# Kernel tuning notes

Measured on AMD Instinct MI355X. Metric: run time of the kernel, lower is better.

## Reference

```python
import jax, jax.numpy as jnp
import numpy as np

N_RAYS = 4096
N_SAMPLES = 128
NEAR, FAR = 0.5, 4.0
BOX_MIN, BOX_MAX = -4.0, 4.0
N_LEVELS = 16
F_PER_LEVEL = 2
LOG2_T = 19
LOW_RES, HIGH_RES = 16.0, 512.0
GEO_FEAT = 15
HIDDEN = 64
HIDDEN_C = 64
IN_CH = N_LEVELS * F_PER_LEVEL      # 32 hash-grid features
IN_CH_VIEWS = 16                     # SH degree 4
OUT_CH = 4                           # 3 color channels + sigma (last)
N_APP = 64
APP_DIM = 16

PRIMES = np.array([1, 2654435761, 805459861], dtype=np.uint32)
OFFSETS = np.array([[i, j, k] for i in (0, 1) for j in (0, 1) for k in (0, 1)], dtype=np.int32)  # [8,3]

C0 = 0.28209479177387814
C1 = 0.4886025119029199
C2 = (1.0925484305920792, -1.0925484305920792, 0.31539156525252005, -1.0925484305920792, 0.5462742152960396)
C3 = (-0.5900435899266435, 2.890611442640554, -0.4570457994644658, 0.3731763325901154, -0.4570457994644658, 1.445305721320277, -0.5900435899266435)


def sh_encode(d):
    x, y, z = d[..., 0], d[..., 1], d[..., 2]
    xx, yy, zz = x * x, y * y, z * z
    xy, yz, xz = x * y, y * z, x * z
    return jnp.stack([
        C0 * jnp.ones_like(x),
        -C1 * y, C1 * z, -C1 * x,
        C2[0] * xy, C2[1] * yz, C2[2] * (2 * zz - xx - yy), C2[3] * xz, C2[4] * (xx - yy),
        C3[0] * y * (3 * xx - yy), C3[1] * xy * z, C3[2] * y * (4 * zz - xx - yy),
        C3[3] * z * (2 * zz - 3 * xx - 3 * yy), C3[4] * x * (4 * zz - xx - yy),
        C3[5] * z * (xx - yy), C3[6] * x * (xx - 3 * yy)], axis=-1)


def hash_encode(x, tables):
    # x: [N,3]; tables: [L, 2^T, F]. Multi-res hash grid with trilinear interp (Instant-NGP / HashNeRF).
    keep = jnp.all((x >= BOX_MIN) & (x <= BOX_MAX), axis=-1)
    xc = jnp.clip(x, BOX_MIN, BOX_MAX)
    b = np.exp((np.log(HIGH_RES) - np.log(LOW_RES)) / (N_LEVELS - 1))
    resolutions = jnp.asarray(np.floor(LOW_RES * b ** np.arange(N_LEVELS)), dtype=jnp.float32)
    hmask = jnp.uint32(2 ** LOG2_T - 1)
    primes = jnp.asarray(PRIMES)
    off = jnp.asarray(OFFSETS)
    off_u = off.astype(jnp.uint32)

    def level(args):
        table, res = args
        grid = (BOX_MAX - BOX_MIN) / res
        pos = (xc - BOX_MIN) / grid
        bl = jnp.floor(pos)
        frac = pos - bl                                    # [N,3]
        corners = bl.astype(jnp.uint32)[:, None, :] + off_u[None]  # [N,8,3]
        h = corners * primes                               # uint32 wraparound
        idx = (h[..., 0] ^ h[..., 1] ^ h[..., 2]) & hmask  # [N,8]
        emb = table[idx]                                   # [N,8,F]
        w = jnp.stack([1.0 - frac, frac], axis=-1)         # [N,3,2]
        cw = w[:, 0, off[:, 0]] * w[:, 1, off[:, 1]] * w[:, 2, off[:, 2]]  # [N,8]
        return jnp.einsum('nc,ncf->nf', cw, emb)           # [N,F]

    feats = jax.lax.map(level, (tables, resolutions))      # [L,N,F]
    feats = jnp.transpose(feats, (1, 0, 2)).reshape(x.shape[0], -1)
    return feats, keep


def _forward(rays, hash_tables, w_s0, w_s1, w_s2, w_c0, w_c1, w_c2, w_c3, app_table):
    R = rays.shape[0]
    rays_o, rays_d = rays[:, :3], rays[:, 3:6]
    codes = rays[:, 6].astype(jnp.int32)
    z = jnp.linspace(NEAR, FAR, N_SAMPLES)
    zvals = jax.lax.stop_gradient(jnp.broadcast_to(z, (R, N_SAMPLES)))
    samples = jax.lax.stop_gradient(rays_o[:, None, :] + rays_d[:, None, :] * z[None, :, None])  # [R,S,3]
    viewdirs = jax.lax.stop_gradient(jnp.broadcast_to(rays_d[:, None, :], (R, N_SAMPLES, 3)))

    pts = samples.reshape(-1, 3)
    dirs = viewdirs.reshape(-1, 3)
    enc_p, keep = hash_encode(pts, hash_tables)            # [N,32], [N]
    enc_d = sh_encode(dirs)                                # [N,16]

    # sigma network (bias-free, HashNeRF NeRFSmall)
    h = jax.nn.relu(enc_p @ w_s0)
    h = jax.nn.relu(h @ w_s1)
    h = h @ w_s2                                           # [N, 1+geo_feat]
    sigma = h[:, :1]
    geo = h[:, 1:]

    # color network with per-ray appearance embedding
    app = app_table[jnp.repeat(codes, N_SAMPLES)]          # [N, APP_DIM]
    c = jnp.concatenate([enc_d, geo, app], axis=-1)
    c = jax.nn.relu(c @ w_c0)
    c = jax.nn.relu(c @ w_c1)
    c = jax.nn.relu(c @ w_c2)
    c = c @ w_c3                                           # [N, OUT_CH-1]

    sigma = jnp.where(keep[:, None], sigma, 0.0)           # output[~keep_mask, -1] = 0
    raw = jnp.concatenate([c, sigma], axis=-1).reshape(R, N_SAMPLES, OUT_CH)

    # volumetric integration
    dists = jnp.concatenate([zvals[:, 1:] - zvals[:, :-1], jnp.full((R, 1), 1e10)], axis=-1)
    dists = dists * jnp.linalg.norm(rays_d, axis=-1, keepdims=True)
    sig = jax.nn.relu(raw[..., -1])
    alpha = 1.0 - jnp.exp(-sig * dists)
    trans = jnp.cumprod(jnp.concatenate([jnp.ones((R, 1)), 1.0 - alpha + 1e-10], axis=-1), axis=-1)[:, :-1]
    weights = alpha * trans                                # [R,S]
    chs = jax.nn.sigmoid(raw[..., :-1])
    chs_map = jnp.einsum('rs,rsc->rc', weights, chs)       # [R, OUT_CH-1]
    depth_map = jnp.sum(weights * zvals, axis=-1)          # [R]
    p = jnp.concatenate([weights, 1.0 - jnp.sum(weights, -1, keepdims=True) + 1e-6], axis=-1)
    p = jnp.clip(p, 1e-12, None)
    p = p / jnp.sum(p, -1, keepdims=True)
    sparsity_loss = -jnp.sum(p * jnp.log(p), axis=-1)      # [R] Categorical entropy
    return chs_map, depth_map, sparsity_loss


def setup_inputs() -> dict:
    key = jax.random.key(0)
    ks = jax.random.split(key, 12)
    rays_o = jax.random.uniform(ks[0], (N_RAYS, 3), minval=-0.5, maxval=0.5)
    d = jax.random.normal(ks[1], (N_RAYS, 3))
    rays_d = d / jnp.linalg.norm(d, axis=-1, keepdims=True)
    codes = jax.random.randint(ks[2], (N_RAYS, 1), 0, N_APP).astype(jnp.float32)
    rays = jnp.concatenate([rays_o, rays_d, codes], axis=-1)  # [R,7]
    hash_tables = (jax.random.uniform(ks[3], (N_LEVELS, 2 ** LOG2_T, F_PER_LEVEL)) * 2.0 - 1.0) * 1e-4
    def init_w(k, shape):
        return jax.random.normal(k, shape) * (1.0 / np.sqrt(shape[0]))
    w_s0 = init_w(ks[4], (IN_CH, HIDDEN))
    w_s1 = init_w(ks[5], (HIDDEN, HIDDEN))
    w_s2 = init_w(ks[6], (HIDDEN, 1 + GEO_FEAT))
    c_in = IN_CH_VIEWS + GEO_FEAT + APP_DIM
    w_c0 = init_w(ks[7], (c_in, HIDDEN_C))
    w_c1 = init_w(ks[8], (HIDDEN_C, HIDDEN_C))
    w_c2 = init_w(ks[9], (HIDDEN_C, HIDDEN_C))
    w_c3 = init_w(ks[10], (HIDDEN_C, OUT_CH - 1))
    app_table = jax.random.normal(ks[11], (N_APP, APP_DIM)) * 0.01
    return {"rays": rays, "app_code": 0, "hash_tables": hash_tables,
            "w_s0": w_s0, "w_s1": w_s1, "w_s2": w_s2,
            "w_c0": w_c0, "w_c1": w_c1, "w_c2": w_c2, "w_c3": w_c3,
            "app_table": app_table}


def reference(rays, app_code, hash_tables, w_s0, w_s1, w_s2, w_c0, w_c1, w_c2, w_c3, app_table):
    # app_code arg is ignored by the original forward (it re-reads rays[:, 6]).
    return _forward(rays, hash_tables, w_s0, w_s1, w_s2, w_c0, w_c1, w_c2, w_c3, app_table)
```

## Files before the change

kernel.cpp:

```cpp
#include <hip/hip_runtime.h>
#include <math.h>

typedef unsigned short u16;
typedef short bf16x8 __attribute__((ext_vector_type(8)));
typedef float f32x4 __attribute__((ext_vector_type(4)));

#define NRAYS 4096
#define NSAMP 128
#define NPTS (NRAYS * NSAMP)
#define TBL_MASK 0x7FFFFu
#define LVL_STRIDE (524288 * 2)

#define WB_C0 0
#define WB_C1 4096
#define WB_C2 8192
#define WB_C3 12288
#define RAW_OFF 65536

#define MEMBAR() asm volatile("" ::: "memory")

struct ResArr { float r[16]; };

__device__ __forceinline__ u16 f2b(float f) {
  unsigned u = __float_as_uint(f);
  unsigned r = u + 0x7FFFu + ((u >> 16) & 1u);
  return (u16)(r >> 16);
}
__device__ __forceinline__ unsigned pack2(float lo, float hi) {
  return (unsigned)f2b(lo) | ((unsigned)f2b(hi) << 16);
}
__device__ __forceinline__ float b2f(u16 u) {
  return __uint_as_float(((unsigned)u) << 16);
}
__device__ __forceinline__ float sigmoidf_(float x) { return 1.f / (1.f + expf(-x)); }

template<int IN, int OUT>
__device__ __forceinline__ void layer(const float (&in)[IN], float (&out)[OUT],
                                      const float* __restrict__ W, bool dorelu)
{
  constexpr int CH = (OUT < 32) ? OUT : 32;
  #pragma unroll
  for (int oc = 0; oc < OUT; oc += CH) {
    float acc[CH];
    #pragma unroll
    for (int o = 0; o < CH; ++o) acc[o] = 0.f;
    #pragma unroll
    for (int i = 0; i < IN; ++i) {
      const float x = in[i];
      const float* wr = W + i * OUT + oc;
      #pragma unroll
      for (int o = 0; o < CH; ++o) acc[o] = fmaf(x, wr[o], acc[o]);
    }
    #pragma unroll
    for (int o = 0; o < CH; ++o) out[oc + o] = dorelu ? fmaxf(acc[o], 0.f) : acc[o];
  }
}

__global__ void __launch_bounds__(256)
prep_kernel(const float* __restrict__ wc0, const float* __restrict__ wc1,
            const float* __restrict__ wc2, const float* __restrict__ wc3,
            u16* __restrict__ wb)
{
  __shared__ int P[32];
  __shared__ int Pinv[32];
  const int t = threadIdx.x;
  if (t < 64) {
    const int g = t >> 4;
    for (int tt = 0; tt < 32; ++tt) {
      bf16x8 A, B;
      #pragma unroll
      for (int e = 0; e < 8; ++e) {
        A[e] = (short)f2b((float)(g * 8 + e + 1));
        B[e] = (short)((g * 8 + e == tt) ? 0x3F80 : 0);
      }
      f32x4 c = {0.f, 0.f, 0.f, 0.f};
      c = __builtin_amdgcn_mfma_f32_16x16x32_bf16(A, B, c, 0, 0, 0);
      if (t == 0) P[tt] = (int)(c[0] + 0.5f) - 1;
    }
  }
  __syncthreads();
  if (t < 32) Pinv[t] = t;
  __syncthreads();
  if (t < 32) { int p = P[t]; if (p >= 0 && p < 32) Pinv[p] = t; }
  __syncthreads();

  for (int i = t; i < 4096; i += 256) {
    int o = i >> 6, s6 = i & 63, kt = (s6 & 32) | Pinv[s6 & 31];
    wb[WB_C0 + i] = f2b(kt < 47 ? wc0[kt * 64 + o] : 0.f);
  }
  for (int i = t; i < 4096; i += 256) {
    int o = i >> 6, s6 = i & 63, kt = (s6 & 32) | Pinv[s6 & 31];
    wb[WB_C1 + i] = f2b(wc1[kt * 64 + o]);
  }
  for (int i = t; i < 4096; i += 256) {
    int o = i >> 6, s6 = i & 63, kt = (s6 & 32) | Pinv[s6 & 31];
    wb[WB_C2 + i] = f2b(wc2[kt * 64 + o]);
  }
  for (int i = t; i < 1024; i += 256) {
    int o = i >> 6, s6 = i & 63, kt = (s6 & 32) | Pinv[s6 & 31];
    wb[WB_C3 + i] = f2b(o < 3 ? wc3[kt * 3 + o] : 0.f);
  }
}

__global__ void __launch_bounds__(256, 4)
point_kernel(const float* __restrict__ rays, const float* __restrict__ tables,
             const float* __restrict__ ws0, const float* __restrict__ ws1,
             const float* __restrict__ ws2, const u16* __restrict__ wb,
             const float* __restrict__ app_table, u16* __restrict__ raw, ResArr RES)
{
  __shared__ char lds[4 * 8192 + 4 * 64 * 4];
  const int t = threadIdx.x, wv = t >> 6, lane = t & 63;
  char* buf = lds + wv * 8192;
  float* sigb = (float*)(lds + 32768 + wv * 256);
  const int pBase = blockIdx.x * 256 + wv * 64;
  const int q = lane & 15, g = lane >> 4;
  const unsigned fswz = (unsigned)((q & 7) << 4);
  const unsigned myswz = (unsigned)((lane & 7) << 4);

  const int ptG = pBase + lane;
  const int r = ptG >> 7, s = ptG & (NSAMP - 1);
  const float ox = rays[r * 7 + 0], oy = rays[r * 7 + 1], oz = rays[r * 7 + 2];
  const float dx = rays[r * 7 + 3], dy = rays[r * 7 + 4], dz = rays[r * 7 + 5];
  const int code = (int)rays[r * 7 + 6];
  const float z = 0.5f + (3.5f / 127.f) * (float)s;
  const float x = fmaf(dx, z, ox), y = fmaf(dy, z, oy), w = fmaf(dz, z, oz);
  const bool keep = (x >= -4.f && x <= 4.f && y >= -4.f && y <= 4.f &&
                     w >= -4.f && w <= 4.f);
  const float xc = fminf(fmaxf(x, -4.f), 4.f);
  const float yc = fminf(fmaxf(y, -4.f), 4.f);
  const float zc = fminf(fmaxf(w, -4.f), 4.f);

  float encp[32];
  #pragma unroll
  for (int l = 0; l < 16; ++l) {
    const float res = RES.r[l];
    const float sc = res * 0.125f;
    const float px = (xc + 4.f) * sc, py = (yc + 4.f) * sc, pz = (zc + 4.f) * sc;
    const float bx = floorf(px), by = floorf(py), bz = floorf(pz);
    const float fx = px - bx, fy = py - by, fz = pz - bz;
    const unsigned ix = (unsigned)bx, iy = (unsigned)by, iz = (unsigned)bz;
    const unsigned hx0 = ix, hx1 = ix + 1u;
    const unsigned hy0 = iy * 2654435761u, hy1 = (iy + 1u) * 2654435761u;
    const unsigned hz0 = iz * 805459861u,  hz1 = (iz + 1u) * 805459861u;
    const float wx0 = 1.f - fx, wy0 = 1.f - fy, wz0 = 1.f - fz;
    const float* tl = tables + (size_t)l * LVL_STRIDE;
    float f0 = 0.f, f1 = 0.f;
    #pragma unroll
    for (int c = 0; c < 8; ++c) {
      const unsigned cx = (c >> 2) & 1, cy = (c >> 1) & 1, cz = c & 1;
      const unsigned idx = ((cx ? hx1 : hx0) ^ (cy ? hy1 : hy0) ^ (cz ? hz1 : hz0)) & TBL_MASK;
      const float cw = (cx ? fx : wx0) * (cy ? fy : wy0) * (cz ? fz : wz0);
      const float2 e = *reinterpret_cast<const float2*>(tl + (size_t)idx * 2);
      f0 = fmaf(cw, e.x, f0);
      f1 = fmaf(cw, e.y, f1);
    }
    encp[2 * l] = f0;
    encp[2 * l + 1] = f1;
  }

  float h1[64]; layer<32, 64>(encp, h1, ws0, true);
  float h2[64]; layer<64, 64>(h1, h2, ws1, true);
  float gg[16]; layer<64, 16>(h2, gg, ws2, false);
  sigb[lane] = keep ? gg[0] : 0.f;

  {
    float cin[64];
    const float xx = dx * dx, yy = dy * dy, zz2 = dz * dz;
    const float xy = dx * dy, yz = dy * dz, xz = dx * dz;
    cin[0]  = 0.28209479177387814f;
    cin[1]  = -0.4886025119029199f * dy;
    cin[2]  = 0.4886025119029199f * dz;
    cin[3]  = -0.4886025119029199f * dx;
    cin[4]  = 1.0925484305920792f * xy;
    cin[5]  = -1.0925484305920792f * yz;
    cin[6]  = 0.31539156525252005f * (2.f * zz2 - xx - yy);
    cin[7]  = -1.0925484305920792f * xz;
    cin[8]  = 0.5462742152960396f * (xx - yy);
    cin[9]  = -0.5900435899266435f * dy * (3.f * xx - yy);
    cin[10] = 2.890611442640554f * xy * dz;
    cin[11] = -0.4570457994644658f * dy * (4.f * zz2 - xx - yy);
    cin[12] = 0.3731763325901154f * dz * (2.f * zz2 - 3.f * xx - 3.f * yy);
    cin[13] = -0.4570457994644658f * dx * (4.f * zz2 - xx - yy);
    cin[14] = 1.445305721320277f * dz * (xx - yy);
    cin[15] = -0.5900435899266435f * dx * (xx - 3.f * yy);
    #pragma unroll
    for (int i = 0; i < 15; ++i) cin[16 + i] = gg[1 + i];
    const float4* ap = (const float4*)(app_table + (size_t)code * 16);
    float4 a0 = ap[0], a1 = ap[1], a2 = ap[2], a3 = ap[3];
    cin[31] = a0.x; cin[32] = a0.y; cin[33] = a0.z; cin[34] = a0.w;
    cin[35] = a1.x; cin[36] = a1.y; cin[37] = a1.z; cin[38] = a1.w;
    cin[39] = a2.x; cin[40] = a2.y; cin[41] = a2.z; cin[42] = a2.w;
    cin[43] = a3.x; cin[44] = a3.y; cin[45] = a3.z; cin[46] = a3.w;
    #pragma unroll
    for (int i = 47; i < 64; ++i) cin[i] = 0.f;
    #pragma unroll
    for (int c = 0; c < 8; ++c) {
      uint4 u;
      u.x = pack2(cin[8 * c + 0], cin[8 * c + 1]);
      u.y = pack2(cin[8 * c + 2], cin[8 * c + 3]);
      u.z = pack2(cin[8 * c + 4], cin[8 * c + 5]);
      u.w = pack2(cin[8 * c + 6], cin[8 * c + 7]);
      *(uint4*)(buf + lane * 128 + (((unsigned)(c * 16)) ^ myswz)) = u;
    }
  }
  MEMBAR();

  auto rdB = [&](int n, int kc) -> bf16x8 {
    return *(const bf16x8*)(buf + (n * 16 + q) * 128 + (((unsigned)(kc * 64 + g * 16)) ^ fswz));
  };
  auto ldA = [&](const u16* Wp, int row, int kc) -> bf16x8 {
    return *(const bf16x8*)(Wp + row * 64 + kc * 32 + g * 8);
  };
  auto wrC = [&](int n, int slot0, f32x4 c) {
    c[0] = fmaxf(c[0], 0.f); c[1] = fmaxf(c[1], 0.f);
    c[2] = fmaxf(c[2], 0.f); c[3] = fmaxf(c[3], 0.f);
    uint2 u; u.x = pack2(c[0], c[1]); u.y = pack2(c[2], c[3]);
    *(uint2*)(buf + (n * 16 + q) * 128 + (((unsigned)(slot0 * 2)) ^ fswz)) = u;
  };

  auto layer64 = [&](const u16* Wp) {
    bf16x8 A[4][2];
    #pragma unroll
    for (int m = 0; m < 4; ++m) {
      A[m][0] = ldA(Wp, m * 16 + q, 0);
      A[m][1] = ldA(Wp, m * 16 + q, 1);
    }
    #pragma unroll
    for (int n = 0; n < 4; ++n) {
      bf16x8 b0 = rdB(n, 0), b1 = rdB(n, 1);
      #pragma unroll
      for (int m = 0; m < 4; ++m) {
        f32x4 c = f32x4{0.f, 0.f, 0.f, 0.f};
        c = __builtin_amdgcn_mfma_f32_16x16x32_bf16(A[m][0], b0, c, 0, 0, 0);
        c = __builtin_amdgcn_mfma_f32_16x16x32_bf16(A[m][1], b1, c, 0, 0, 0);
        wrC(n, m * 16 + g * 4, c);
      }
    }
    MEMBAR();
  };

  layer64(wb + WB_C0);
  layer64(wb + WB_C1);
  layer64(wb + WB_C2);

  {
    const u16* Wp = wb + WB_C3;
    bf16x8 A0 = ldA(Wp, q, 0), A1 = ldA(Wp, q, 1);
    #pragma unroll
    for (int n = 0; n < 4; ++n) {
      bf16x8 b0 = rdB(n, 0), b1 = rdB(n, 1);
      f32x4 c = f32x4{0.f, 0.f, 0.f, 0.f};
      c = __builtin_amdgcn_mfma_f32_16x16x32_bf16(A0, b0, c, 0, 0, 0);
      c = __builtin_amdgcn_mfma_f32_16x16x32_bf16(A1, b1, c, 0, 0, 0);
      if (g == 0) {
        uint2 o; o.x = pack2(c[0], c[1]); o.y = pack2(c[2], sigb[n * 16 + q]);
        *(uint2*)(raw + (size_t)(pBase + n * 16 + q) * 4) = o;
      }
    }
  }
}

__global__ void __launch_bounds__(256)
render_kernel(const float* __restrict__ rays, const u16* __restrict__ raw,
              float* __restrict__ out)
{
  const int r = blockIdx.x * 256 + threadIdx.x;
  if (r >= NRAYS) return;
  const float dx = rays[r * 7 + 3], dy = rays[r * 7 + 4], dz = rays[r * 7 + 5];
  const float nrm = sqrtf(dx * dx + dy * dy + dz * dz);
  const float dstep = 3.5f / 127.f;
  const ushort4* rp = reinterpret_cast<const ushort4*>(raw) + (size_t)r * NSAMP;

  float T = 1.f, sumw = 0.f, sumwz = 0.f, cm0 = 0.f, cm1 = 0.f, cm2 = 0.f;
  for (int s = 0; s < NSAMP; ++s) {
    const ushort4 rw = rp[s];
    const float dist = ((s < NSAMP - 1) ? dstep : 1e10f) * nrm;
    const float sigv = fmaxf(b2f(rw.w), 0.f);
    const float alpha = 1.f - expf(-sigv * dist);
    const float wgt = alpha * T;
    T *= (1.f - alpha + 1e-10f);
    const float zv = 0.5f + dstep * (float)s;
    sumw += wgt;
    sumwz = fmaf(wgt, zv, sumwz);
    cm0 = fmaf(wgt, sigmoidf_(b2f(rw.x)), cm0);
    cm1 = fmaf(wgt, sigmoidf_(b2f(rw.y)), cm1);
    cm2 = fmaf(wgt, sigmoidf_(b2f(rw.z)), cm2);
  }

  float S1 = 0.f, S2 = 0.f, T2 = 1.f;
  for (int s = 0; s < NSAMP; ++s) {
    const ushort4 rw = rp[s];
    const float dist = ((s < NSAMP - 1) ? dstep : 1e10f) * nrm;
    const float sigv = fmaxf(b2f(rw.w), 0.f);
    const float alpha = 1.f - expf(-sigv * dist);
    const float wgt = alpha * T2;
    T2 *= (1.f - alpha + 1e-10f);
    const float qv = fmaxf(wgt, 1e-12f);
    S1 += qv;
    S2 = fmaf(qv, logf(qv), S2);
  }
  const float plast = fmaxf(1.f - sumw + 1e-6f, 1e-12f);
  S1 += plast;
  S2 = fmaf(plast, logf(plast), S2);
  const float ent = logf(S1) - S2 / S1;

  out[r * 3 + 0] = cm0;
  out[r * 3 + 1] = cm1;
  out[r * 3 + 2] = cm2;
  out[NRAYS * 3 + r] = sumwz;
  out[NRAYS * 4 + r] = ent;
}

extern "C" void kernel_launch(void* const* d_in, const int* in_sizes, int n_in,
                              void* d_out, int out_size, void* d_ws, size_t ws_size,
                              hipStream_t stream)
{
  const float* rays   = (const float*)d_in[0];
  const float* tables = (const float*)d_in[2];
  const float* ws0    = (const float*)d_in[3];
  const float* ws1    = (const float*)d_in[4];
  const float* ws2    = (const float*)d_in[5];
  const float* wc0    = (const float*)d_in[6];
  const float* wc1    = (const float*)d_in[7];
  const float* wc2    = (const float*)d_in[8];
  const float* wc3    = (const float*)d_in[9];
  const float* app    = (const float*)d_in[10];

  u16* wb  = (u16*)d_ws;
  u16* raw = (u16*)((char*)d_ws + RAW_OFF);
  float* out = (float*)d_out;

  ResArr RES;
  const double b = exp((log(512.0) - log(16.0)) / 15.0);
  for (int l = 0; l < 16; ++l) RES.r[l] = (float)floor(16.0 * pow(b, (double)l));

  hipLaunchKernelGGL(prep_kernel, dim3(1), dim3(256), 0, stream,
                     wc0, wc1, wc2, wc3, wb);
  hipLaunchKernelGGL(point_kernel, dim3(NPTS / 256), dim3(256), 0, stream,
                     rays, tables, ws0, ws1, ws2, wb, app, raw, RES);
  hipLaunchKernelGGL(render_kernel, dim3(16), dim3(256), 0, stream,
                     rays, raw, out);
}
```

Baseline: 279.4 us.

## Move sigma MLP to MFMA with three-way bf16 split emulating fp32

The density MLP (32→64→64→16), previously evaluated with scalar fp32 FMAs per thread, now runs on bf16 MFMA. Weights and activations are each split into high/mid/low bf16 parts so the sum of cross products approximates fp32 accuracy. The geo-feature output is written straight into the LDS color-input buffer, with the color weights remapped around the sigma slot. This replaces heavy VALU work and register pressure with six-term MFMA passes and more LDS round-trips, and occupancy is lowered to 3 waves-blocks.

```diff
diff --git a/kernel.cpp b/kernel.cpp
--- a/kernel.cpp
+++ b/kernel.cpp
@@ -11,15 +11,25 @@
 #define TBL_MASK 0x7FFFFu
 #define LVL_STRIDE (524288 * 2)
 
-#define WB_C0 0
-#define WB_C1 4096
-#define WB_C2 8192
-#define WB_C3 12288
-#define RAW_OFF 65536
+#define SB_W0H 0
+#define SB_W0M 2048
+#define SB_W0L 4096
+#define SB_W1H 6144
+#define SB_W1M 10240
+#define SB_W1L 14336
+#define SB_W2H 18432
+#define SB_W2M 19456
+#define SB_W2L 20480
+#define WB_C0 21504
+#define WB_C1 25600
+#define WB_C2 29696
+#define WB_C3 33792
+#define RAW_OFF 131072
 
 #define MEMBAR() asm volatile("" ::: "memory")
 
 struct ResArr { float r[16]; };
+template<int N> struct IC { static constexpr int value = N; };
 
 __device__ __forceinline__ u16 f2b(float f) {
   unsigned u = __float_as_uint(f);
@@ -32,34 +42,22 @@
 __device__ __forceinline__ float b2f(u16 u) {
   return __uint_as_float(((unsigned)u) << 16);
 }
+template<int SP>
+__device__ __forceinline__ u16 splitb(float x) {
+  u16 h = f2b(x);
+  if (SP == 0) return h;
+  float r = x - b2f(h);
+  u16 m = f2b(r);
+  if (SP == 1) return m;
+  return f2b(r - b2f(m));
+}
 __device__ __forceinline__ float sigmoidf_(float x) { return 1.f / (1.f + expf(-x)); }
 
-template<int IN, int OUT>
-__device__ __forceinline__ void layer(const float (&in)[IN], float (&out)[OUT],
-                                      const float* __restrict__ W, bool dorelu)
-{
-  constexpr int CH = (OUT < 32) ? OUT : 32;
-  #pragma unroll
-  for (int oc = 0; oc < OUT; oc += CH) {
-    float acc[CH];
-    #pragma unroll
-    for (int o = 0; o < CH; ++o) acc[o] = 0.f;
-    #pragma unroll
-    for (int i = 0; i < IN; ++i) {
-      const float x = in[i];
-      const float* wr = W + i * OUT + oc;
-      #pragma unroll
-      for (int o = 0; o < CH; ++o) acc[o] = fmaf(x, wr[o], acc[o]);
-    }
-    #pragma unroll
-    for (int o = 0; o < CH; ++o) out[oc + o] = dorelu ? fmaxf(acc[o], 0.f) : acc[o];
-  }
-}
-
 __global__ void __launch_bounds__(256)
-prep_kernel(const float* __restrict__ wc0, const float* __restrict__ wc1,
-            const float* __restrict__ wc2, const float* __restrict__ wc3,
-            u16* __restrict__ wb)
+prep_kernel(const float* __restrict__ ws0, const float* __restrict__ ws1,
+            const float* __restrict__ ws2, const float* __restrict__ wc0,
+            const float* __restrict__ wc1, const float* __restrict__ wc2,
+            const float* __restrict__ wc3, u16* __restrict__ wb)
 {
   __shared__ int P[32];
   __shared__ int Pinv[32];
@@ -84,34 +82,81 @@
   if (t < 32) { int p = P[t]; if (p >= 0 && p < 32) Pinv[p] = t; }
   __syncthreads();
 
+  for (int i = t; i < 2048; i += 256) {
+    int o = i >> 5, k = i & 31, kt = Pinv[k];
+    float v = ws0[kt * 64 + o];
+    u16 h = f2b(v); float r = v - b2f(h); u16 m = f2b(r); u16 l = f2b(r - b2f(m));
+    wb[SB_W0H + i] = h; wb[SB_W0M + i] = m; wb[SB_W0L + i] = l;
+  }
   for (int i = t; i < 4096; i += 256) {
-    int o = i >> 6, s6 = i & 63, kt = (s6 & 32) | Pinv[s6 & 31];
-    wb[WB_C0 + i] = f2b(kt < 47 ? wc0[kt * 64 + o] : 0.f);
+    int o = i >> 6, k = i & 63, kt = (k & 32) | Pinv[k & 31];
+    float v = ws1[kt * 64 + o];
+    u16 h = f2b(v); float r = v - b2f(h); u16 m = f2b(r); u16 l = f2b(r - b2f(m));
+    wb[SB_W1H + i] = h; wb[SB_W1M + i] = m; wb[SB_W1L + i] = l;
+  }
+  for (int i = t; i < 1024; i += 256) {
+    int o = i >> 6, k = i & 63, kt = (k & 32) | Pinv[k & 31];
+    float v = ws2[kt * 16 + o];
+    u16 h = f2b(v); float r = v - b2f(h); u16 m = f2b(r); u16 l = f2b(r - b2f(m));
+    wb[SB_W2H + i] = h; wb[SB_W2M + i] = m; wb[SB_W2L + i] = l;
   }
   for (int i = t; i < 4096; i += 256) {
-    int o = i >> 6, s6 = i & 63, kt = (s6 & 32) | Pinv[s6 & 31];
+    int o = i >> 6, s = i & 63, kt = (s & 32) | Pinv[s & 31];
+    float v = 0.f;
+    if (kt < 16) v = wc0[kt * 64 + o];
+    else if (kt >= 17 && kt <= 47) v = wc0[(kt - 1) * 64 + o];
+    wb[WB_C0 + i] = f2b(v);
+  }
+  for (int i = t; i < 4096; i += 256) {
+    int o = i >> 6, s = i & 63, kt = (s & 32) | Pinv[s & 31];
     wb[WB_C1 + i] = f2b(wc1[kt * 64 + o]);
   }
   for (int i = t; i < 4096; i += 256) {
-    int o = i >> 6, s6 = i & 63, kt = (s6 & 32) | Pinv[s6 & 31];
+    int o = i >> 6, s = i & 63, kt = (s & 32) | Pinv[s & 31];
     wb[WB_C2 + i] = f2b(wc2[kt * 64 + o]);
   }
   for (int i = t; i < 1024; i += 256) {
-    int o = i >> 6, s6 = i & 63, kt = (s6 & 32) | Pinv[s6 & 31];
+    int o = i >> 6, s = i & 63, kt = (s & 32) | Pinv[s & 31];
     wb[WB_C3 + i] = f2b(o < 3 ? wc3[kt * 3 + o] : 0.f);
   }
 }
 
-__global__ void __launch_bounds__(256, 4)
+template<int NM, int NKC, int NASP>
+__device__ __forceinline__ void sigma_pass(const char* buf, const u16* __restrict__ wb,
+                                           int offH, int offM, int offL,
+                                           f32x4 (&acc)[4][NM], int q, int g, unsigned fswz)
+{
+  #pragma unroll
+  for (int n = 0; n < 4; ++n) {
+    bf16x8 b[NKC];
+    #pragma unroll
+    for (int kc = 0; kc < NKC; ++kc)
+      b[kc] = *(const bf16x8*)(buf + (n * 16 + q) * 128 + (((unsigned)(kc * 64 + g * 16)) ^ fswz));
+    #pragma unroll
+    for (int m = 0; m < NM; ++m) {
+      const int arow = (NM == 1 ? q : m * 16 + q);
+      #pragma unroll
+      for (int asp = 0; asp < NASP; ++asp) {
+        const u16* Wp = wb + (asp == 0 ? offH : (asp == 1 ? offM : offL));
+        #pragma unroll
+        for (int kc = 0; kc < NKC; ++kc) {
+          bf16x8 A = *(const bf16x8*)(Wp + arow * (NKC * 32) + kc * 32 + g * 8);
+          acc[n][m] = __builtin_amdgcn_mfma_f32_16x16x32_bf16(A, b[kc], acc[n][m], 0, 0, 0);
+        }
+      }
+    }
+  }
+}
+
+__global__ void __launch_bounds__(256, 3)
 point_kernel(const float* __restrict__ rays, const float* __restrict__ tables,
-             const float* __restrict__ ws0, const float* __restrict__ ws1,
-             const float* __restrict__ ws2, const u16* __restrict__ wb,
-             const float* __restrict__ app_table, u16* __restrict__ raw, ResArr RES)
+             const u16* __restrict__ wb, const float* __restrict__ app_table,
+             u16* __restrict__ raw, ResArr RES)
 {
-  __shared__ char lds[4 * 8192 + 4 * 64 * 4];
+  __shared__ char lds[4 * 8192 + 4 * 256];
   const int t = threadIdx.x, wv = t >> 6, lane = t & 63;
   char* buf = lds + wv * 8192;
-  float* sigb = (float*)(lds + 32768 + wv * 256);
+  float* keepb = (float*)(lds + 32768 + wv * 256);
   const int pBase = blockIdx.x * 256 + wv * 64;
   const int q = lane & 15, g = lane >> 4;
   const unsigned fswz = (unsigned)((q & 7) << 4);
@@ -157,51 +202,124 @@
     encp[2 * l] = f0;
     encp[2 * l + 1] = f1;
   }
-
-  float h1[64]; layer<32, 64>(encp, h1, ws0, true);
-  float h2[64]; layer<64, 64>(h1, h2, ws1, true);
-  float gg[16]; layer<64, 16>(h2, gg, ws2, false);
-  sigb[lane] = keep ? gg[0] : 0.f;
+  keepb[lane] = keep ? 1.f : 0.f;
+
+  auto fillEnc = [&](auto SPc) {
+    constexpr int SP = decltype(SPc)::value;
+    #pragma unroll
+    for (int c = 0; c < 4; ++c) {
+      uint4 u;
+      u.x = (unsigned)splitb<SP>(encp[8 * c + 0]) | ((unsigned)splitb<SP>(encp[8 * c + 1]) << 16);
+      u.y = (unsigned)splitb<SP>(encp[8 * c + 2]) | ((unsigned)splitb<SP>(encp[8 * c + 3]) << 16);
+      u.z = (unsigned)splitb<SP>(encp[8 * c + 4]) | ((unsigned)splitb<SP>(encp[8 * c + 5]) << 16);
+      u.w = (unsigned)splitb<SP>(encp[8 * c + 6]) | ((unsigned)splitb<SP>(encp[8 * c + 7]) << 16);
+      *(uint4*)(buf + lane * 128 + (((unsigned)(c * 16)) ^ myswz)) = u;
+    }
+  };
+  auto fillC = [&](const f32x4 (&a)[4][4], auto SPc) {
+    constexpr int SP = decltype(SPc)::value;
+    #pragma unroll
+    for (int n = 0; n < 4; ++n)
+      #pragma unroll
+      for (int m = 0; m < 4; ++m) {
+        uint2 u;
+        u.x = (unsigned)splitb<SP>(a[n][m][0]) | ((unsigned)splitb<SP>(a[n][m][1]) << 16);
+        u.y = (unsigned)splitb<SP>(a[n][m][2]) | ((unsigned)splitb<SP>(a[n][m][3]) << 16);
+        *(uint2*)(buf + (n * 16 + q) * 128 + (((unsigned)(m * 32 + g * 8)) ^ fswz)) = u;
+      }
+  };
+
+  f32x4 acc0[4][4];
+  #pragma unroll
+  for (int n = 0; n < 4; ++n)
+    #pragma unroll
+    for (int m = 0; m < 4; ++m) acc0[n][m] = f32x4{0.f, 0.f, 0.f, 0.f};
+
+  fillEnc(IC<0>{}); MEMBAR();
+  sigma_pass<4, 1, 3>(buf, wb, SB_W0H, SB_W0M, SB_W0L, acc0, q, g, fswz); MEMBAR();
+  fillEnc(IC<1>{}); MEMBAR();
+  sigma_pass<4, 1, 2>(buf, wb, SB_W0H, SB_W0M, SB_W0L, acc0, q, g, fswz); MEMBAR();
+  fillEnc(IC<2>{}); MEMBAR();
+  sigma_pass<4, 1, 1>(buf, wb, SB_W0H, SB_W0M, SB_W0L, acc0, q, g, fswz); MEMBAR();
+  #pragma unroll
+  for (int n = 0; n < 4; ++n)
+    #pragma unroll
+    for (int m = 0; m < 4; ++m)
+      #pragma unroll
+      for (int j = 0; j < 4; ++j) acc0[n][m][j] = fmaxf(acc0[n][m][j], 0.f);
+
+  f32x4 acc1[4][4];
+  #pragma unroll
+  for (int n = 0; n < 4; ++n)
+    #pragma unroll
+    for (int m = 0; m < 4; ++m) acc1[n][m] = f32x4{0.f, 0.f, 0.f, 0.f};
+
+  fillC(acc0, IC<0>{}); MEMBAR();
+  sigma_pass<4, 2, 3>(buf, wb, SB_W1H, SB_W1M, SB_W1L, acc1, q, g, fswz); MEMBAR();
+  fillC(acc0, IC<1>{}); MEMBAR();
+  sigma_pass<4, 2, 2>(buf, wb, SB_W1H, SB_W1M, SB_W1L, acc1, q, g, fswz); MEMBAR();
+  fillC(acc0, IC<2>{}); MEMBAR();
+  sigma_pass<4, 2, 1>(buf, wb, SB_W1H, SB_W1M, SB_W1L, acc1, q, g, fswz); MEMBAR();
+  #pragma unroll
+  for (int n = 0; n < 4; ++n)
+    #pragma unroll
+    for (int m = 0; m < 4; ++m)
+      #pragma unroll
+      for (int j = 0; j < 4; ++j) acc1[n][m][j] = fmaxf(acc1[n][m][j], 0.f);
+
+  f32x4 acc2[4][1];
+  #pragma unroll
+  for (int n = 0; n < 4; ++n) acc2[n][0] = f32x4{0.f, 0.f, 0.f, 0.f};
+
+  fillC(acc1, IC<0>{}); MEMBAR();
+  sigma_pass<1, 2, 3>(buf, wb, SB_W2H, SB_W2M, SB_W2L, acc2, q, g, fswz); MEMBAR();
+  fillC(acc1, IC<1>{}); MEMBAR();
+  sigma_pass<1, 2, 2>(buf, wb, SB_W2H, SB_W2M, SB_W2L, acc2, q, g, fswz); MEMBAR();
+  fillC(acc1, IC<2>{}); MEMBAR();
+  sigma_pass<1, 2, 1>(buf, wb, SB_W2H, SB_W2M, SB_W2L, acc2, q, g, fswz); MEMBAR();
+
+  float sigv[4];
+  #pragma unroll
+  for (int n = 0; n < 4; ++n) {
+    sigv[n] = acc2[n][0][0] * keepb[n * 16 + q];
+    uint2 u;
+    u.x = pack2(acc2[n][0][0], acc2[n][0][1]);
+    u.y = pack2(acc2[n][0][2], acc2[n][0][3]);
+    *(uint2*)(buf + (n * 16 + q) * 128 + (((unsigned)(32 + 8 * g)) ^ fswz)) = u;
+  }
 
   {
-    float cin[64];
     const float xx = dx * dx, yy = dy * dy, zz2 = dz * dz;
     const float xy = dx * dy, yz = dy * dz, xz = dx * dz;
-    cin[0]  = 0.28209479177387814f;
-    cin[1]  = -0.4886025119029199f * dy;
-    cin[2]  = 0.4886025119029199f * dz;
-    cin[3]  = -0.4886025119029199f * dx;
-    cin[4]  = 1.0925484305920792f * xy;
-    cin[5]  = -1.0925484305920792f * yz;
-    cin[6]  = 0.31539156525252005f * (2.f * zz2 - xx - yy);
-    cin[7]  = -1.0925484305920792f * xz;
-    cin[8]  = 0.5462742152960396f * (xx - yy);
-    cin[9]  = -0.5900435899266435f * dy * (3.f * xx - yy);
-    cin[10] = 2.890611442640554f * xy * dz;
-    cin[11] = -0.4570457994644658f * dy * (4.f * zz2 - xx - yy);
-    cin[12] = 0.3731763325901154f * dz * (2.f * zz2 - 3.f * xx - 3.f * yy);
-    cin[13] = -0.4570457994644658f * dx * (4.f * zz2 - xx - yy);
-    cin[14] = 1.445305721320277f * dz * (xx - yy);
-    cin[15] = -0.5900435899266435f * dx * (xx - 3.f * yy);
-    #pragma unroll
-    for (int i = 0; i < 15; ++i) cin[16 + i] = gg[1 + i];
+    float e0 = 0.28209479177387814f;
+    float e1 = -0.4886025119029199f * dy;
+    float e2 = 0.4886025119029199f * dz;
+    float e3 = -0.4886025119029199f * dx;
+    float e4 = 1.0925484305920792f * xy;
+    float e5 = -1.0925484305920792f * yz;
+    float e6 = 0.31539156525252005f * (2.f * zz2 - xx - yy);
+    float e7 = -1.0925484305920792f * xz;
+    float e8 = 0.5462742152960396f * (xx - yy);
+    float e9 = -0.5900435899266435f * dy * (3.f * xx - yy);
+    float e10 = 2.890611442640554f * xy * dz;
+    float e11 = -0.4570457994644658f * dy * (4.f * zz2 - xx - yy);
+    float e12 = 0.3731763325901154f * dz * (2.f * zz2 - 3.f * xx - 3.f * yy);
+    float e13 = -0.4570457994644658f * dx * (4.f * zz2 - xx - yy);
+    float e14 = 1.445305721320277f * dz * (xx - yy);
+    float e15 = -0.5900435899266435f * dx * (xx - 3.f * yy);
+    uint4 u0; u0.x = pack2(e0, e1);  u0.y = pack2(e2, e3);  u0.z = pack2(e4, e5);  u0.w = pack2(e6, e7);
+    uint4 u1; u1.x = pack2(e8, e9);  u1.y = pack2(e10, e11); u1.z = pack2(e12, e13); u1.w = pack2(e14, e15);
+    *(uint4*)(buf + lane * 128 + (0u ^ myswz)) = u0;
+    *(uint4*)(buf + lane * 128 + (16u ^ myswz)) = u1;
     const float4* ap = (const float4*)(app_table + (size_t)code * 16);
     float4 a0 = ap[0], a1 = ap[1], a2 = ap[2], a3 = ap[3];
-    cin[31] = a0.x; cin[32] = a0.y; cin[33] = a0.z; cin[34] = a0.w;
-    cin[35] = a1.x; cin[36] = a1.y; cin[37] = a1.z; cin[38] = a1.w;
-    cin[39] = a2.x; cin[40] = a2.y; cin[41] = a2.z; cin[42] = a2.w;
-    cin[43] = a3.x; cin[44] = a3.y; cin[45] = a3.z; cin[46] = a3.w;
-    #pragma unroll
-    for (int i = 47; i < 64; ++i) cin[i] = 0.f;
-    #pragma unroll
-    for (int c = 0; c < 8; ++c) {
-      uint4 u;
-      u.x = pack2(cin[8 * c + 0], cin[8 * c + 1]);
-      u.y = pack2(cin[8 * c + 2], cin[8 * c + 3]);
-      u.z = pack2(cin[8 * c + 4], cin[8 * c + 5]);
-      u.w = pack2(cin[8 * c + 6], cin[8 * c + 7]);
-      *(uint4*)(buf + lane * 128 + (((unsigned)(c * 16)) ^ myswz)) = u;
-    }
+    uint4 v0; v0.x = pack2(a0.x, a0.y); v0.y = pack2(a0.z, a0.w); v0.z = pack2(a1.x, a1.y); v0.w = pack2(a1.z, a1.w);
+    uint4 v1; v1.x = pack2(a2.x, a2.y); v1.y = pack2(a2.z, a2.w); v1.z = pack2(a3.x, a3.y); v1.w = pack2(a3.z, a3.w);
+    *(uint4*)(buf + lane * 128 + (64u ^ myswz)) = v0;
+    *(uint4*)(buf + lane * 128 + (80u ^ myswz)) = v1;
+    uint4 zv; zv.x = 0u; zv.y = 0u; zv.z = 0u; zv.w = 0u;
+    *(uint4*)(buf + lane * 128 + (96u ^ myswz)) = zv;
+    *(uint4*)(buf + lane * 128 + (112u ^ myswz)) = zv;
   }
   MEMBAR();
 
@@ -217,7 +335,6 @@
     uint2 u; u.x = pack2(c[0], c[1]); u.y = pack2(c[2], c[3]);
     *(uint2*)(buf + (n * 16 + q) * 128 + (((unsigned)(slot0 * 2)) ^ fswz)) = u;
   };
-
   auto layer64 = [&](const u16* Wp) {
     bf16x8 A[4][2];
     #pragma unroll
@@ -253,7 +370,7 @@
       c = __builtin_amdgcn_mfma_f32_16x16x32_bf16(A0, b0, c, 0, 0, 0);
       c = __builtin_amdgcn_mfma_f32_16x16x32_bf16(A1, b1, c, 0, 0, 0);
       if (g == 0) {
-        uint2 o; o.x = pack2(c[0], c[1]); o.y = pack2(c[2], sigb[n * 16 + q]);
+        uint2 o; o.x = pack2(c[0], c[1]); o.y = pack2(c[2], sigv[n]);
         *(uint2*)(raw + (size_t)(pBase + n * 16 + q) * 4) = o;
       }
     }
@@ -335,9 +452,9 @@
   for (int l = 0; l < 16; ++l) RES.r[l] = (float)floor(16.0 * pow(b, (double)l));
 
   hipLaunchKernelGGL(prep_kernel, dim3(1), dim3(256), 0, stream,
-                     wc0, wc1, wc2, wc3, wb);
+                     ws0, ws1, ws2, wc0, wc1, wc2, wc3, wb);
   hipLaunchKernelGGL(point_kernel, dim3(NPTS / 256), dim3(256), 0, stream,
-                     rays, tables, ws0, ws1, ws2, wb, app, raw, RES);
+                     rays, tables, wb, app, raw, RES);
   hipLaunchKernelGGL(render_kernel, dim3(16), dim3(256), 0, stream,
                      rays, raw, out);
 }
```

Measured after the change: 575.4 us. +106.0%, slower.
